# Optimization experiments

Hardware: AMD Instinct MI355X
Metric: run time of the kernel (lower is better)

## Reference

```python
import jax, jax.numpy as jnp
import numpy as np

DIM = 512
HEADS = 16
WS = 7  # window size (cube), N = WS**3 = 343
B_ = 128
N = WS ** 3
TABLE = (2 * WS - 1) ** 3  # 2197


def _relative_position_index():
    coords = np.stack(np.meshgrid(np.arange(WS), np.arange(WS), np.arange(WS), indexing='ij'))  # [3,WS,WS,WS]
    cf = coords.reshape(3, -1)  # [3, N]
    rel = cf[:, :, None] - cf[:, None, :]  # [3, N, N]
    rel = rel.transpose(1, 2, 0).copy()
    rel[:, :, 0] += WS - 1
    rel[:, :, 1] += WS - 1
    rel[:, :, 2] += WS - 1
    rel[:, :, 0] *= (2 * WS - 1) * (2 * WS - 1)
    rel[:, :, 1] *= 2 * WS - 1
    return jnp.asarray(rel.sum(-1), dtype=jnp.int32)  # [N, N]


def setup_inputs() -> dict:
    key = jax.random.key(0)
    ks = jax.random.split(key, 8)
    x = jax.random.normal(ks[0], (B_, N, DIM), dtype=jnp.float32)
    q_global = jax.random.normal(ks[1], (1, DIM), dtype=jnp.float32)
    qkv_w = jax.random.normal(ks[2], (3 * DIM, DIM), dtype=jnp.float32) * (DIM ** -0.5)
    qkv_b = jax.random.normal(ks[3], (3 * DIM,), dtype=jnp.float32) * 0.02
    proj_w = jax.random.normal(ks[4], (DIM, DIM), dtype=jnp.float32) * (DIM ** -0.5)
    proj_b = jax.random.normal(ks[5], (DIM,), dtype=jnp.float32) * 0.02
    rel_bias_table = jax.random.normal(ks[6], (TABLE, HEADS), dtype=jnp.float32) * 0.02
    rel_pos_index = _relative_position_index()
    return {"x": x, "q_global": q_global, "qkv_w": qkv_w, "qkv_b": qkv_b,
            "rel_bias_table": rel_bias_table, "proj_w": proj_w, "proj_b": proj_b,
            "rel_pos_index": rel_pos_index}


def reference(x, q_global, qkv_w, qkv_b, rel_bias_table, proj_w, proj_b, rel_pos_index):
    B, Nt, C = x.shape
    hd = C // HEADS
    scale = hd ** -0.5
    # QKV projection (torch Linear: x @ W.T + b)
    qkv = (x @ qkv_w.T + qkv_b).reshape(B, Nt, 3, HEADS, hd)
    qkv = jnp.transpose(qkv, (2, 0, 3, 1, 4))  # [3, B, H, N, hd]
    q, k, v = qkv[0] * scale, qkv[1], qkv[2]
    attn = jnp.einsum('bhqd,bhkd->bhqk', q, k)  # [B, H, N, N]
    # relative position bias gather: table[idx] -> [N, N, H] -> [H, N, N]
    bias = rel_bias_table[rel_pos_index.reshape(-1)].reshape(Nt, Nt, HEADS)
    attn = attn + jnp.transpose(bias, (2, 0, 1))[None]
    attn = jax.nn.softmax(attn, axis=-1)
    out = jnp.einsum('bhqk,bhkd->bhqd', attn, v)  # [B, H, N, hd]
    out = jnp.transpose(out, (0, 2, 1, 3)).reshape(B, Nt, C)
    return out @ proj_w.T + proj_b
```

## Files before the change

### kernel.cpp

```cpp
#include <hip/hip_runtime.h>

typedef unsigned short u16;
typedef __attribute__((ext_vector_type(8))) short short8;
typedef __attribute__((ext_vector_type(4))) float f32x4;
typedef __attribute__((ext_vector_type(16))) float f32x16;
typedef __attribute__((ext_vector_type(4))) unsigned uint4v;

#define NTOK 343
#define DIMC 512
#define HEADS_ 16
#define BATCH 128
#define MROWS 43904
#define TBL 117649

#define LOG2E 1.4426950408889634f
#define QSCALE (0.17677669529663687f * LOG2E)

__device__ __forceinline__ u16 f2bf(float f) {
  unsigned u = __builtin_bit_cast(unsigned, f);
  unsigned r = (u + 0x7fffu + ((u >> 16) & 1u)) >> 16;
  return (u16)r;
}
__device__ __forceinline__ float bf2f(u16 x) {
  return __builtin_bit_cast(float, ((unsigned)x) << 16);
}
__device__ __forceinline__ unsigned cvtpk(float lo, float hi) {
  unsigned r;
  asm("v_cvt_pk_bf16_f32 %0, %1, %2" : "=v"(r) : "v"(lo), "v"(hi));
  return r;
}

__global__ void cvt_f32_bf16_k(const float* __restrict__ in, u16* __restrict__ out, int n4) {
  int i = blockIdx.x * blockDim.x + threadIdx.x;
  int st = gridDim.x * blockDim.x;
  for (; i < n4; i += st) {
    float4 v = reinterpret_cast<const float4*>(in)[i];
    ushort4 o;
    o.x = f2bf(v.x); o.y = f2bf(v.y); o.z = f2bf(v.z); o.w = f2bf(v.w);
    reinterpret_cast<ushort4*>(out)[i] = o;
  }
}

__global__ void bias_pre_k(const float* __restrict__ table, const int* __restrict__ idx,
                           u16* __restrict__ biasB) {
  int t = blockIdx.x * 256 + threadIdx.x;
  if (t >= HEADS_ * 121 * 256) return;
  int r4 = t & 3;
  int l = (t >> 2) & 63;
  int rest = t >> 8;
  int tq = rest % 11;
  int nt = (rest / 11) % 11;
  int h = rest / 121;
  int q = tq * 32 + (l & 31);
  int hi = l >> 5;
  ushort4 o;
  u16* oe = (u16*)&o;
#pragma unroll
  for (int rr = 0; rr < 4; ++rr) {
    int r = r4 * 4 + rr;
    int tok = nt * 32 + (r & 3) + 8 * (r >> 2) + 4 * hi;
    float v = (q < NTOK && tok < NTOK) ? (LOG2E * table[idx[q * NTOK + tok] * HEADS_ + h])
                                       : -1e30f;
    oe[rr] = f2bf(v);
  }
  *reinterpret_cast<ushort4*>(biasB +
                              (size_t)(((h * 11 + nt) * 11 + tq) * 1024 + l * 16 + r4 * 4)) = o;
}

#define GLD16(gptr, lptr)                                                        \
  __builtin_amdgcn_global_load_lds(                                              \
      (const __attribute__((address_space(1))) void*)(const void*)(gptr),        \
      (__attribute__((address_space(3))) void*)(void*)(lptr), 16, 0, 0)

template <int EPI>
__global__ __launch_bounds__(256) void gemm_bt_k(const u16* __restrict__ A,
                                                 const u16* __restrict__ B,
                                                 const float* __restrict__ bias,
                                                 void* __restrict__ C, int N, int K) {
  const int NBL = N >> 7;
  int nwg = gridDim.x;
  int orig = blockIdx.x;
  int qq = nwg >> 3, rr = nwg & 7;
  int xcd = orig & 7, lid = orig >> 3;
  int bid = (xcd < rr ? xcd * (qq + 1) : rr * (qq + 1) + (xcd - rr) * qq) + lid;
  int mb = bid / NBL, nb = bid % NBL;
  __shared__ __align__(16) u16 As[2][128 * 64];
  __shared__ __align__(16) u16 Bs[2][128 * 64];
  int tid = threadIdx.x;
  int w = tid >> 6, l = tid & 63;
  int wr = w >> 1, wc = w & 1;
  f32x4 acc[4][4];
#pragma unroll
  for (int i = 0; i < 4; i++)
#pragma unroll
    for (int j = 0; j < 4; j++) acc[i][j] = (f32x4){0.f, 0.f, 0.f, 0.f};

  const int l8r = l >> 3, l8c = l & 7;
  const int woff = (w * 32) * 64;

#define STG2(kt, slot)                                                                    \
  {                                                                                       \
    _Pragma("unroll") for (int i4 = 0; i4 < 4; ++i4) {                                    \
      int rowl = w * 32 + i4 * 8 + l8r;                                                   \
      int cbs = (l8c * 16) ^ (((rowl >> 1) & 7) << 4);                                    \
      GLD16(A + (size_t)(mb * 128 + rowl) * K + (kt)*64 + (cbs >> 1),                     \
            As[slot] + woff + i4 * 512 + l * 8);                                          \
      GLD16(B + (size_t)(nb * 128 + rowl) * K + (kt)*64 + (cbs >> 1),                     \
            Bs[slot] + woff + i4 * 512 + l * 8);                                          \
    }                                                                                     \
  }

  int KT = K >> 6;
  STG2(0, 0);
  __syncthreads();
  for (int kt = 0; kt < KT; ++kt) {
    int cur = kt & 1;
    if (kt + 1 < KT) STG2(kt + 1, cur ^ 1);
#pragma unroll
    for (int kk = 0; kk < 2; ++kk) {
      short8 af[4], bf[4];
#pragma unroll
      for (int i = 0; i < 4; i++) {
        int off = (wr * 64 + i * 16 + (l & 15)) * 128 + kk * 64 + (l >> 4) * 16;
        off ^= ((off >> 8) & 7) << 4;
        af[i] = *reinterpret_cast<const short8*>((const u16*)As[cur] + (off >> 1));
      }
#pragma unroll
      for (int j = 0; j < 4; j++) {
        int off = (wc * 64 + j * 16 + (l & 15)) * 128 + kk * 64 + (l >> 4) * 16;
        off ^= ((off >> 8) & 7) << 4;
        bf[j] = *reinterpret_cast<const short8*>((const u16*)Bs[cur] + (off >> 1));
      }
#pragma unroll
      for (int i = 0; i < 4; i++)
#pragma unroll
        for (int j = 0; j < 4; j++)
          acc[i][j] = __builtin_amdgcn_mfma_f32_16x16x32_bf16(af[i], bf[j], acc[i][j], 0, 0, 0);
    }
    __syncthreads();
  }
#undef STG2

  int r0 = mb * 128 + wr * 64 + (l >> 4) * 4;
  int c0 = nb * 128 + wc * 64 + (l & 15);
#pragma unroll
  for (int j = 0; j < 4; j++) {
    int col = c0 + j * 16;
    float bv = bias[col];
    float mul = (EPI == 0 && col < 512) ? QSCALE : 1.0f;
#pragma unroll
    for (int i = 0; i < 4; i++) {
      int row = r0 + i * 16;
      if (EPI == 0) {
        u16* Cp = (u16*)C + (size_t)row * N + col;
#pragma unroll
        for (int r = 0; r < 4; r += 2) {
          unsigned pk = cvtpk((acc[i][j][r] + bv) * mul, (acc[i][j][r + 1] + bv) * mul);
          Cp[(size_t)r * N] = (u16)pk;
          Cp[(size_t)(r + 1) * N] = (u16)(pk >> 16);
        }
      } else {
#pragma unroll
        for (int r = 0; r < 4; r++)
          ((float*)C)[(size_t)(row + r) * N + col] = acc[i][j][r] + bv;
      }
    }
  }
}

__global__ __launch_bounds__(256, 3) void attn_k(const u16* __restrict__ qkv,
                                                 const u16* __restrict__ biasB,
                                                 u16* __restrict__ outA) {
  int p = blockIdx.x;
  int jj = p >> 3;
  int h = 2 * (p & 7) + (jj >> 7);
  int b = jj & 127;
  __shared__ __align__(16) u16 kS[352 * 40];
  __shared__ __align__(16) u16 vT[32 * 370];
  int tid = threadIdx.x;

  for (int idx = tid; idx < 352 * 4; idx += 256) {
    int row = idx >> 2, seg = idx & 3;
    uint4 vk = {0, 0, 0, 0};
    if (row < NTOK)
      vk = *reinterpret_cast<const uint4*>(qkv + (size_t)(b * NTOK + row) * 1536 + 512 +
                                           h * 32 + seg * 8);
    *reinterpret_cast<uint4*>(kS + row * 40 + seg * 8) = vk;
  }
  for (int idx = tid; idx < NTOK * 4; idx += 256) {
    int row = idx >> 2, seg = idx & 3;
    size_t base = (size_t)(b * NTOK + row) * 1536 + 1024 + h * 32 + seg * 8;
    uint4 vv = *reinterpret_cast<const uint4*>(qkv + base);
    const u16* e = reinterpret_cast<const u16*>(&vv);
#pragma unroll
    for (int t = 0; t < 8; ++t) vT[(seg * 8 + t) * 370 + row] = e[t];
  }
  for (int idx = tid; idx < 32 * 9; idx += 256) vT[(idx / 9) * 370 + NTOK + (idx % 9)] = 0;
  __syncthreads();

  int w = tid >> 6, l = tid & 63;
  const int d32 = l & 31, hi = l >> 5;
  const bool upHalf = (hi != 0);

  for (int tq = w; tq < 11; tq += 4) {
    int qrow = tq * 32 + d32;
    short8 bq0 = (short8){0, 0, 0, 0, 0, 0, 0, 0};
    short8 bq1 = (short8){0, 0, 0, 0, 0, 0, 0, 0};
    if (qrow < NTOK) {
      const u16* qb = qkv + (size_t)(b * NTOK + qrow) * 1536 + h * 32 + hi * 8;
      bq0 = *reinterpret_cast<const short8*>(qb);
      bq1 = *reinterpret_cast<const short8*>(qb + 16);
    }
    f32x16 O = {0, 0, 0, 0, 0, 0, 0, 0, 0, 0, 0, 0, 0, 0, 0, 0};
    float tot = 0.f;
    const u16* bbase = biasB + ((size_t)(h * 121 + tq)) * 1024 + l * 16;
    for (int nt = 0; nt < 11; ++nt) {
      const u16* kr = kS + (nt * 32 + d32) * 40 + hi * 8;
      short8 ak0 = *reinterpret_cast<const short8*>(kr);
      short8 ak1 = *reinterpret_cast<const short8*>(kr + 16);
      f32x16 S = {0, 0, 0, 0, 0, 0, 0, 0, 0, 0, 0, 0, 0, 0, 0, 0};
      S = __builtin_amdgcn_mfma_f32_32x32x16_bf16(ak0, bq0, S, 0, 0, 0);
      S = __builtin_amdgcn_mfma_f32_32x32x16_bf16(ak1, bq1, S, 0, 0, 0);
      const u16* bp = bbase + (size_t)nt * 11 * 1024;
      short8 bb0 = *reinterpret_cast<const short8*>(bp);
      short8 bb1 = *reinterpret_cast<const short8*>(bp + 8);
      float ex[16];
#pragma unroll
      for (int r = 0; r < 16; ++r) {
        u16 bw = (u16)((r < 8) ? bb0[r] : bb1[r - 8]);
        float v = S[r] + bf2f(bw);
        ex[r] = __builtin_amdgcn_exp2f(v);
        tot += ex[r];
      }
      unsigned W[8];
#pragma unroll
      for (int r2 = 0; r2 < 8; ++r2) W[r2] = cvtpk(ex[2 * r2], ex[2 * r2 + 1]);
#pragma unroll
      for (int c = 0; c < 2; ++c) {
        unsigned x0 = W[4 * c + 0], x1 = W[4 * c + 1];
        unsigned y0 = W[4 * c + 2], y1 = W[4 * c + 3];
        unsigned x0s = (unsigned)__shfl_xor((int)x0, 32);
        unsigned x1s = (unsigned)__shfl_xor((int)x1, 32);
        unsigned y0s = (unsigned)__shfl_xor((int)y0, 32);
        unsigned y1s = (unsigned)__shfl_xor((int)y1, 32);
        uint4v ap;
        ap.x = upHalf ? y0s : x0;
        ap.y = upHalf ? y1s : x1;
        ap.z = upHalf ? y0 : x0s;
        ap.w = upHalf ? y1 : x1s;
        short8 bv = *reinterpret_cast<const short8*>(vT + d32 * 370 + nt * 32 + c * 16 + hi * 8);
        O = __builtin_amdgcn_mfma_f32_32x32x16_bf16(__builtin_bit_cast(short8, ap), bv, O,
                                                    0, 0, 0);
      }
    }
    tot += __builtin_bit_cast(float, __shfl_xor(__builtin_bit_cast(int, tot), 32));
    float inv = 1.0f / tot;
#pragma unroll
    for (int r = 0; r < 16; ++r) {
      int qloc = (r & 3) + 8 * (r >> 2) + 4 * hi;
      float ir = __shfl(inv, qloc);
      int q = tq * 32 + qloc;
      if (q < NTOK) {
        float ov = O[r] * ir;
        outA[(size_t)(b * NTOK + q) * 512 + h * 32 + d32] = (u16)cvtpk(ov, ov);
      }
    }
  }
}

extern "C" void kernel_launch(void* const* d_in, const int* in_sizes, int n_in,
                              void* d_out, int out_size, void* d_ws, size_t ws_size,
                              hipStream_t stream) {
  const float* x      = (const float*)d_in[0];
  const float* qkv_w  = (const float*)d_in[2];
  const float* qkv_b  = (const float*)d_in[3];
  const float* table  = (const float*)d_in[4];
  const float* proj_w = (const float*)d_in[5];
  const float* proj_b = (const float*)d_in[6];
  const int*   relidx = (const int*)d_in[7];

  char* ws = (char*)d_ws;
  u16*   x_bf  = (u16*)(ws);
  u16*   qw_bf = (u16*)(ws + 44957696);
  u16*   pw_bf = (u16*)(ws + 46530560);
  u16*   qkv_o = (u16*)(ws + 47054848);
  u16*   biasB = (u16*)(ws + 181927936);

  cvt_f32_bf16_k<<<2048, 256, 0, stream>>>(x, x_bf, (BATCH * NTOK * DIMC) / 4);
  cvt_f32_bf16_k<<<768, 256, 0, stream>>>(qkv_w, qw_bf, (3 * DIMC * DIMC) / 4);
  cvt_f32_bf16_k<<<256, 256, 0, stream>>>(proj_w, pw_bf, (DIMC * DIMC) / 4);
  bias_pre_k<<<1936, 256, 0, stream>>>(table, relidx, biasB);

  gemm_bt_k<0><<<343 * 12, 256, 0, stream>>>(x_bf, qw_bf, qkv_b, qkv_o, 1536, 512);
  attn_k<<<BATCH * HEADS_, 256, 0, stream>>>(qkv_o, biasB, x_bf);
  gemm_bt_k<1><<<343 * 4, 256, 0, stream>>>(x_bf, pw_bf, proj_b, d_out, 512, 512);
}
```

Before: 263.1 us.

## Software-pipeline QK^T MFMA in attention and merge weight/bias prep kernels

In the attention kernel, the score MFMAs and bias loads for the next key tile are issued before the exp/PV work of the current tile, so matrix-core latency can overlap with the softmax VALU work. The separate weight-conversion and bias-precompute launches are merged into a single prep kernel to remove two launches. The pipelining raises register pressure (an extra f32x16 accumulator plus bias vectors), which could lower occupancy.

```diff
diff --git a/kernel.cpp b/kernel.cpp
--- a/kernel.cpp
+++ b/kernel.cpp
@@ -41,9 +41,22 @@
   }
 }
 
-__global__ void bias_pre_k(const float* __restrict__ table, const int* __restrict__ idx,
-                           u16* __restrict__ biasB) {
-  int t = blockIdx.x * 256 + threadIdx.x;
+__global__ void prep_k(const float* __restrict__ qw, u16* __restrict__ qwb,
+                       const float* __restrict__ pw, u16* __restrict__ pwb,
+                       const float* __restrict__ table, const int* __restrict__ idx,
+                       u16* __restrict__ biasB) {
+  int bidx = blockIdx.x;
+  if (bidx < 1024) {
+    const float* in = bidx < 768 ? qw : pw;
+    u16* out = bidx < 768 ? qwb : pwb;
+    int i = (bidx < 768 ? bidx : bidx - 768) * 256 + threadIdx.x;
+    float4 v = reinterpret_cast<const float4*>(in)[i];
+    ushort4 o;
+    o.x = f2bf(v.x); o.y = f2bf(v.y); o.z = f2bf(v.z); o.w = f2bf(v.w);
+    reinterpret_cast<ushort4*>(out)[i] = o;
+    return;
+  }
+  int t = (bidx - 1024) * 256 + threadIdx.x;
   if (t >= HEADS_ * 121 * 256) return;
   int r4 = t & 3;
   int l = (t >> 2) & 63;
@@ -102,7 +115,7 @@
   {                                                                                       \
     _Pragma("unroll") for (int i4 = 0; i4 < 4; ++i4) {                                    \
       int rowl = w * 32 + i4 * 8 + l8r;                                                   \
-      int cbs = (l8c * 16) ^ (((rowl >> 1) & 7) << 4);                                    \
+      int cbs = (l8c * 16) ^ (((rowl >> 1) & 7) << 4);     \
       GLD16(A + (size_t)(mb * 128 + rowl) * K + (kt)*64 + (cbs >> 1),                     \
             As[slot] + woff + i4 * 512 + l * 8);                                          \
       GLD16(B + (size_t)(nb * 128 + rowl) * K + (kt)*64 + (cbs >> 1),                     \
@@ -201,6 +214,7 @@
   int w = tid >> 6, l = tid & 63;
   const int d32 = l & 31, hi = l >> 5;
   const bool upHalf = (hi != 0);
+  const f32x16 z16 = {0, 0, 0, 0, 0, 0, 0, 0, 0, 0, 0, 0, 0, 0, 0, 0};
 
   for (int tq = w; tq < 11; tq += 4) {
     int qrow = tq * 32 + d32;
@@ -211,19 +225,35 @@
       bq0 = *reinterpret_cast<const short8*>(qb);
       bq1 = *reinterpret_cast<const short8*>(qb + 16);
     }
-    f32x16 O = {0, 0, 0, 0, 0, 0, 0, 0, 0, 0, 0, 0, 0, 0, 0, 0};
+    f32x16 O = z16;
     float tot = 0.f;
     const u16* bbase = biasB + ((size_t)(h * 121 + tq)) * 1024 + l * 16;
-    for (int nt = 0; nt < 11; ++nt) {
-      const u16* kr = kS + (nt * 32 + d32) * 40 + hi * 8;
+
+    f32x16 S;
+    short8 bb0, bb1;
+    {
+      const u16* kr = kS + (d32)*40 + hi * 8;
       short8 ak0 = *reinterpret_cast<const short8*>(kr);
       short8 ak1 = *reinterpret_cast<const short8*>(kr + 16);
-      f32x16 S = {0, 0, 0, 0, 0, 0, 0, 0, 0, 0, 0, 0, 0, 0, 0, 0};
-      S = __builtin_amdgcn_mfma_f32_32x32x16_bf16(ak0, bq0, S, 0, 0, 0);
+      S = __builtin_amdgcn_mfma_f32_32x32x16_bf16(ak0, bq0, z16, 0, 0, 0);
       S = __builtin_amdgcn_mfma_f32_32x32x16_bf16(ak1, bq1, S, 0, 0, 0);
-      const u16* bp = bbase + (size_t)nt * 11 * 1024;
-      short8 bb0 = *reinterpret_cast<const short8*>(bp);
-      short8 bb1 = *reinterpret_cast<const short8*>(bp + 8);
+      bb0 = *reinterpret_cast<const short8*>(bbase);
+      bb1 = *reinterpret_cast<const short8*>(bbase + 8);
+    }
+
+    for (int nt = 0; nt < 11; ++nt) {
+      f32x16 Sn = z16;
+      short8 bb0n = bb0, bb1n = bb1;
+      if (nt + 1 < 11) {
+        const u16* krn = kS + ((nt + 1) * 32 + d32) * 40 + hi * 8;
+        short8 a0n = *reinterpret_cast<const short8*>(krn);
+        short8 a1n = *reinterpret_cast<const short8*>(krn + 16);
+        const u16* bpn = bbase + (size_t)(nt + 1) * 11 * 1024;
+        bb0n = *reinterpret_cast<const short8*>(bpn);
+        bb1n = *reinterpret_cast<const short8*>(bpn + 8);
+        Sn = __builtin_amdgcn_mfma_f32_32x32x16_bf16(a0n, bq0, Sn, 0, 0, 0);
+        Sn = __builtin_amdgcn_mfma_f32_32x32x16_bf16(a1n, bq1, Sn, 0, 0, 0);
+      }
       float ex[16];
 #pragma unroll
       for (int r = 0; r < 16; ++r) {
@@ -252,6 +282,9 @@
         O = __builtin_amdgcn_mfma_f32_32x32x16_bf16(__builtin_bit_cast(short8, ap), bv, O,
                                                     0, 0, 0);
       }
+      S = Sn;
+      bb0 = bb0n;
+      bb1 = bb1n;
     }
     tot += __builtin_bit_cast(float, __shfl_xor(__builtin_bit_cast(int, tot), 32));
     float inv = 1.0f / tot;
@@ -287,9 +320,7 @@
   u16*   biasB = (u16*)(ws + 181927936);
 
   cvt_f32_bf16_k<<<2048, 256, 0, stream>>>(x, x_bf, (BATCH * NTOK * DIMC) / 4);
-  cvt_f32_bf16_k<<<768, 256, 0, stream>>>(qkv_w, qw_bf, (3 * DIMC * DIMC) / 4);
-  cvt_f32_bf16_k<<<256, 256, 0, stream>>>(proj_w, pw_bf, (DIMC * DIMC) / 4);
-  bias_pre_k<<<1936, 256, 0, stream>>>(table, relidx, biasB);
+  prep_k<<<2960, 256, 0, stream>>>(qkv_w, qw_bf, proj_w, pw_bf, table, relidx, biasB);
 
   gemm_bt_k<0><<<343 * 12, 256, 0, stream>>>(x_bf, qw_bf, qkv_b, qkv_o, 1536, 512);
   attn_k<<<BATCH * HEADS_, 256, 0, stream>>>(qkv_o, biasB, x_bf);
```

After: 250.3 us. 1.05x faster.
